# Performance work log

Hardware: AMD Instinct MI355X
Metric: run time of the kernel (lower is better)

The kernel has to match this reference:

```python
import jax, jax.numpy as jnp
import numpy as np

B, S, D = 8, 1024, 1152
H, HD = 16, 72  # num_heads, head_dim

def setup_inputs() -> dict:
    key = jax.random.key(0)
    ks = jax.random.split(key, 7)
    hidden_states = jax.random.normal(ks[0], (B, S, D), dtype=jnp.float32)
    cos = jax.random.uniform(ks[1], (S, HD), dtype=jnp.float32)
    sin = jax.random.uniform(ks[2], (S, HD), dtype=jnp.float32)
    qkv_w = jax.random.normal(ks[3], (3 * D, D), dtype=jnp.float32) * 0.02
    qkv_b = jnp.zeros((3 * D,), dtype=jnp.float32)
    proj_w = jax.random.normal(ks[4], (D, D), dtype=jnp.float32) * 0.02
    proj_b = jnp.zeros((D,), dtype=jnp.float32)
    return {"hidden_states": hidden_states, "cos": cos, "sin": sin,
            "qkv_w": qkv_w, "qkv_b": qkv_b, "proj_w": proj_w, "proj_b": proj_b}

def _rotate_half(x):
    x1, x2 = jnp.split(x, 2, axis=-1)
    return jnp.concatenate((-x2, x1), axis=-1)

def reference(hidden_states, cos, sin, qkv_w, qkv_b, proj_w, proj_b):
    b, s, d = hidden_states.shape
    # fused QKV projection
    qkv = hidden_states @ qkv_w.T + qkv_b            # [B,S,3D]
    qkv = qkv.reshape(b, s, 3, H, HD)
    qkv = jnp.transpose(qkv, (2, 0, 3, 1, 4))        # [3,B,H,S,HD]
    q, k, v = qkv[0], qkv[1], qkv[2]
    # rotary embedding, cos/sin broadcast [1,1,S,HD]
    c = cos[None, None, :, :]
    sn = sin[None, None, :, :]
    q = q * c + _rotate_half(q) * sn
    k = k * c + _rotate_half(k) * sn
    # SDPA
    scale = HD ** -0.5
    scores = jnp.einsum('bhqd,bhkd->bhqk', q, k) * scale
    probs = jax.nn.softmax(scores, axis=-1)
    attn = jnp.einsum('bhqk,bhkd->bhqd', probs, v)   # [B,H,S,HD]
    attn = jnp.transpose(attn, (0, 2, 1, 3)).reshape(b, s, d)
    return attn @ proj_w.T + proj_b
```

## Files before the change

kernel.cpp:

```cpp
#include <hip/hip_runtime.h>
#include <hip/hip_bf16.h>


typedef __attribute__((ext_vector_type(8))) short short8;
typedef __attribute__((ext_vector_type(4))) float f32x4;

__device__ __forceinline__ float bflo(unsigned int u) { return __uint_as_float(u << 16); }

__device__ __forceinline__ unsigned int f2bf(float f) {
    unsigned int u = __float_as_uint(f);
    return (u + 0x7FFFu + ((u >> 16) & 1u)) >> 16;
}

__device__ __forceinline__ void stout(float* C, size_t idx, float v) { C[idx] = v; }
__device__ __forceinline__ void stout(__hip_bfloat16* C, size_t idx, float v) {
    C[idx] = __float2bfloat16(v);
}

__device__ __forceinline__ void async_cp16(const void* g, void* l) {
    __builtin_amdgcn_global_load_lds((const __attribute__((address_space(1))) void*)g,
                                     (__attribute__((address_space(3))) void*)l, 16, 0, 0);
}

__global__ void f32_to_bf16_pair(
    const float* __restrict__ s0, unsigned short* __restrict__ d0, int n0_4,
    const float* __restrict__ s1, unsigned short* __restrict__ d1, int n1_4)
{
    int i = blockIdx.x * 256 + threadIdx.x;
    const float* s; unsigned short* d;
    if (i < n0_4) { s = s0; d = d0; }
    else if (i < n0_4 + n1_4) { s = s1; d = d1; i -= n0_4; }
    else return;
    float4 f = ((const float4*)s)[i];
    ushort4 r;
    r.x = (unsigned short)f2bf(f.x);
    r.y = (unsigned short)f2bf(f.y);
    r.z = (unsigned short)f2bf(f.z);
    r.w = (unsigned short)f2bf(f.w);
    ((ushort4*)d)[i] = r;
}

template <typename OT>
__global__ __launch_bounds__(256, 2) void gemm_bt_lds(
    const __hip_bfloat16* __restrict__ A,
    const __hip_bfloat16* __restrict__ B,
    const float* __restrict__ bias,
    OT* __restrict__ C,
    int M, int N, int K)
{
    __shared__ __align__(16) unsigned short As[128 * 32];
    __shared__ __align__(16) unsigned short Bs[128 * 32];

    const int tid  = threadIdx.x;
    const int lane = tid & 63;
    const int w    = tid >> 6;
    const int wr   = w >> 1;
    const int wc   = w & 1;
    const int bm   = blockIdx.y * 128;
    const int bn   = blockIdx.x * 128;

    const int lrow = lane >> 2;
    const int lcol = (lane & 3) * 8;

    const unsigned short* ag[2];
    const unsigned short* bg[2];
    unsigned short* al[2];
    unsigned short* bl[2];
#pragma unroll
    for (int c = 0; c < 2; c++) {
        const int r = w * 32 + c * 16 + lrow;
        ag[c] = (const unsigned short*)A + (size_t)(bm + r) * K + lcol;
        bg[c] = (const unsigned short*)B + (size_t)(bn + r) * K + lcol;
        al[c] = &As[(w * 2 + c) * 512];
        bl[c] = &Bs[(w * 2 + c) * 512];
    }

    f32x4 acc[4][4];
#pragma unroll
    for (int i = 0; i < 4; i++)
#pragma unroll
        for (int j = 0; j < 4; j++)
            acc[i][j] = (f32x4){0.f, 0.f, 0.f, 0.f};

    const int kq = (lane >> 4) * 8;
    const int fr = lane & 15;

    for (int k0 = 0; k0 < K; k0 += 32) {
        __syncthreads();
#pragma unroll
        for (int c = 0; c < 2; c++) {
            async_cp16(ag[c] + k0, al[c]);
            async_cp16(bg[c] + k0, bl[c]);
        }
        __syncthreads();

        short8 af[4], bf[4];
#pragma unroll
        for (int i = 0; i < 4; i++)
            af[i] = *(const short8*)&As[(wr * 64 + i * 16 + fr) * 32 + kq];
#pragma unroll
        for (int j = 0; j < 4; j++)
            bf[j] = *(const short8*)&Bs[(wc * 64 + j * 16 + fr) * 32 + kq];
#pragma unroll
        for (int i = 0; i < 4; i++)
#pragma unroll
            for (int j = 0; j < 4; j++)
                acc[i][j] = __builtin_amdgcn_mfma_f32_16x16x32_bf16(af[i], bf[j], acc[i][j], 0, 0, 0);
    }

#pragma unroll
    for (int i = 0; i < 4; i++) {
        const int mrow = bm + wr * 64 + i * 16 + (lane >> 4) * 4;
#pragma unroll
        for (int j = 0; j < 4; j++) {
            const int ncol = bn + wc * 64 + j * 16 + fr;
            const float bv = bias[ncol];
#pragma unroll
            for (int r = 0; r < 4; r++) {
                stout(C, (size_t)(mrow + r) * N + ncol, acc[i][j][r] + bv);
            }
        }
    }
}

__global__ void rope_qk(
    const __hip_bfloat16* __restrict__ qkv,
    const float* __restrict__ cosp,
    const float* __restrict__ sinp,
    __hip_bfloat16* __restrict__ Qo,
    __hip_bfloat16* __restrict__ Ko)
{
    const int tid = blockIdx.x * 256 + threadIdx.x;
    const int total = 8 * 16 * 1024 * 36;
    if (tid >= total) return;
    const int i    = tid % 36;
    const int rest = tid / 36;
    const int s    = rest & 1023;
    const int bh   = rest >> 10;

    const size_t row = (size_t)((bh >> 4) * 1024 + s) * 3456;
    const int col = (bh & 15) * 72 + i;

    const float c1 = cosp[s * 72 + i];
    const float c2 = cosp[s * 72 + i + 36];
    const float s1 = sinp[s * 72 + i];
    const float s2 = sinp[s * 72 + i + 36];

    const float qa = __bfloat162float(qkv[row + col]);
    const float qb = __bfloat162float(qkv[row + col + 36]);
    const float ka = __bfloat162float(qkv[row + 1152 + col]);
    const float kb = __bfloat162float(qkv[row + 1152 + col + 36]);

    const size_t ob = ((size_t)bh * 1024 + s) * 72 + i;
    const float QS = 0.17002324f;

    Qo[ob]      = __float2bfloat16((qa * c1 - qb * s1) * QS);
    Qo[ob + 36] = __float2bfloat16((qb * c2 + qa * s2) * QS);
    Ko[ob]      = __float2bfloat16(ka * c1 - kb * s1);
    Ko[ob + 36] = __float2bfloat16(kb * c2 + ka * s2);
}

__global__ void v_transpose(
    const __hip_bfloat16* __restrict__ qkv,
    __hip_bfloat16* __restrict__ Vt)
{
    __shared__ __align__(16) unsigned short T[64 * 72];
    const int tid = threadIdx.x;
    const int bh = blockIdx.x >> 4;
    const int st = blockIdx.x & 15;
    const unsigned short* src = (const unsigned short*)qkv
        + ((size_t)(bh >> 4) * 1024 + st * 64) * 3456 + 2304 + (bh & 15) * 72;

#pragma unroll
    for (int k = 0; k < 3; k++) {
        const int c = tid + k * 256;
        if (c < 576) {
            const int s = c / 9, off = (c % 9) * 8;
            *(uint4*)&T[c * 8] = *(const uint4*)(src + (size_t)s * 3456 + off);
        }
    }
    __syncthreads();

    unsigned short* dst = (unsigned short*)Vt + (size_t)(bh * 16 + st) * 72 * 64;
#pragma unroll
    for (int k = 0; k < 9; k++) {
        const int o = tid + k * 256;
        const int d = o >> 5;
        const int sl = (o & 31) * 2;
        ushort2 v;
        v.x = T[sl * 72 + d];
        v.y = T[(sl + 1) * 72 + d];
        *(ushort2*)&dst[d * 64 + sl] = v;
    }
}

__global__ __launch_bounds__(256, 4) void attn_mfma(
    const __hip_bfloat16* __restrict__ Q,
    const __hip_bfloat16* __restrict__ K,
    const __hip_bfloat16* __restrict__ Vt,
    __hip_bfloat16* __restrict__ O)
{
    __shared__ __align__(16) unsigned short Ks[64][72];
    __shared__ __align__(16) unsigned short Vs[80][72];
    __shared__ __align__(16) unsigned short Ps[4][32][72];

    const int tid  = threadIdx.x;
    const int lane = tid & 63;
    const int w    = tid >> 6;
    const int quad = lane >> 4;
    const int fr   = lane & 15;
    const int bh   = blockIdx.x & 127;
    const int qt   = blockIdx.x >> 7;
    const int qbase = qt * 128 + w * 32;

    const short8 z8 = (short8){0,0,0,0,0,0,0,0};

    for (int idx = tid; idx < 8 * 72; idx += 256)
        Vs[72 + idx / 72][idx % 72] = (idx < 72) ? (unsigned short)0x3F80 : (unsigned short)0;

    const unsigned short* qp = (const unsigned short*)Q + ((size_t)bh * 1024 + qbase + fr) * 72;
    short8 qf[2][3];
#pragma unroll
    for (int sub = 0; sub < 2; sub++) {
        const unsigned short* qs = qp + sub * 16 * 72;
        qf[sub][0] = *(const short8*)(qs + quad * 8);
        qf[sub][1] = *(const short8*)(qs + 32 + quad * 8);
        qf[sub][2] = (quad == 0) ? *(const short8*)(qs + 64) : z8;
    }

    f32x4 Oa[2][5];
#pragma unroll
    for (int sub = 0; sub < 2; sub++)
#pragma unroll
        for (int n = 0; n < 5; n++) Oa[sub][n] = (f32x4){0.f, 0.f, 0.f, 0.f};

    const unsigned short* kg0 = (const unsigned short*)K + (size_t)bh * 1024 * 72;
    const unsigned short* vg0 = (const unsigned short*)Vt + (size_t)bh * 16 * 72 * 64;

#pragma unroll 1
    for (int t = 0; t < 16; t++) {
        __syncthreads();
        const unsigned short* kg = kg0 + (size_t)t * 64 * 72;
        const unsigned short* vg = vg0 + (size_t)t * 72 * 64;
#pragma unroll
        for (int k = 0; k < 3; k++) {
            const int c = tid + k * 256;
            if (c < 576) {
                *(uint4*)&((unsigned short*)Ks)[c * 8] = *(const uint4*)(kg + c * 8);
                *(uint4*)&Vs[c >> 3][(c & 7) * 8] = *(const uint4*)(vg + c * 8);
            }
        }
        __syncthreads();

#pragma unroll
        for (int nt = 0; nt < 4; nt++) {
            short8 b0 = *(const short8*)&Ks[nt * 16 + fr][quad * 8];
            short8 b1 = *(const short8*)&Ks[nt * 16 + fr][32 + quad * 8];
            short8 b2 = (quad == 0) ? *(const short8*)&Ks[nt * 16 + fr][64] : z8;
            f32x4 s0 = (f32x4){0.f, 0.f, 0.f, 0.f};
            f32x4 s1 = (f32x4){0.f, 0.f, 0.f, 0.f};
            s0 = __builtin_amdgcn_mfma_f32_16x16x32_bf16(qf[0][0], b0, s0, 0, 0, 0);
            s1 = __builtin_amdgcn_mfma_f32_16x16x32_bf16(qf[1][0], b0, s1, 0, 0, 0);
            s0 = __builtin_amdgcn_mfma_f32_16x16x32_bf16(qf[0][1], b1, s0, 0, 0, 0);
            s1 = __builtin_amdgcn_mfma_f32_16x16x32_bf16(qf[1][1], b1, s1, 0, 0, 0);
            s0 = __builtin_amdgcn_mfma_f32_16x16x32_bf16(qf[0][2], b2, s0, 0, 0, 0);
            s1 = __builtin_amdgcn_mfma_f32_16x16x32_bf16(qf[1][2], b2, s1, 0, 0, 0);
#pragma unroll
            for (int r = 0; r < 4; r++) {
                Ps[w][quad * 4 + r][nt * 16 + fr]      = (unsigned short)f2bf(exp2f(s0[r]));
                Ps[w][16 + quad * 4 + r][nt * 16 + fr] = (unsigned short)f2bf(exp2f(s1[r]));
            }
        }

#pragma unroll
        for (int ks = 0; ks < 2; ks++) {
            short8 ap0 = *(const short8*)&Ps[w][fr][ks * 32 + quad * 8];
            short8 ap1 = *(const short8*)&Ps[w][16 + fr][ks * 32 + quad * 8];
#pragma unroll
            for (int n = 0; n < 5; n++) {
                short8 bv = *(const short8*)&Vs[n * 16 + fr][ks * 32 + quad * 8];
                Oa[0][n] = __builtin_amdgcn_mfma_f32_16x16x32_bf16(ap0, bv, Oa[0][n], 0, 0, 0);
                Oa[1][n] = __builtin_amdgcn_mfma_f32_16x16x32_bf16(ap1, bv, Oa[1][n], 0, 0, 0);
            }
        }
    }

    const int lsrc = (lane & 48) | 8;
    const int b = bh >> 4, h = bh & 15;
    unsigned short* ob = (unsigned short*)O;
#pragma unroll
    for (int sub = 0; sub < 2; sub++) {
        float inv[4];
#pragma unroll
        for (int r = 0; r < 4; r++)
            inv[r] = 1.f / __shfl(Oa[sub][4][r], lsrc, 64);
#pragma unroll
        for (int n = 0; n < 5; n++) {
            const int d = n * 16 + fr;
            if (d < 72) {
#pragma unroll
                for (int r = 0; r < 4; r++) {
                    const size_t idx =
                        ((size_t)b * 1024 + qbase + sub * 16 + quad * 4 + r) * 1152 + h * 72 + d;
                    ob[idx] = (unsigned short)f2bf(Oa[sub][n][r] * inv[r]);
                }
            }
        }
    }
}

extern "C" void kernel_launch(void* const* d_in, const int* in_sizes, int n_in,
                              void* d_out, int out_size, void* d_ws, size_t ws_size,
                              hipStream_t stream)
{
    const float* hs     = (const float*)d_in[0];
    const float* cosp   = (const float*)d_in[1];
    const float* sinp   = (const float*)d_in[2];
    const float* qkv_w  = (const float*)d_in[3];
    const float* qkv_b  = (const float*)d_in[4];
    const float* proj_w = (const float*)d_in[5];
    const float* proj_b = (const float*)d_in[6];
    float* out = (float*)d_out;

    char* ws = (char*)d_ws;
    __hip_bfloat16* qkv_buf = (__hip_bfloat16*)ws;
    __hip_bfloat16* Qb = (__hip_bfloat16*)(ws + 56623104);
    __hip_bfloat16* Kb = Qb + 9437184;
    __hip_bfloat16* Vt = Kb + 9437184;
    __hip_bfloat16* Ab = qkv_buf;

    unsigned short* hs_bf = (unsigned short*)Qb;
    unsigned short* qw_bf = (unsigned short*)Kb;
    unsigned short* pw_bf = (unsigned short*)Qb;

    f32_to_bf16_pair<<<13104, 256, 0, stream>>>(hs, hs_bf, 2359296,
                                                qkv_w, qw_bf, 995328);
    gemm_bt_lds<__hip_bfloat16>
        <<<dim3(27, 64), 256, 0, stream>>>((const __hip_bfloat16*)hs_bf,
                                           (const __hip_bfloat16*)qw_bf,
                                           qkv_b, qkv_buf, 8192, 3456, 1152);
    rope_qk<<<18432, 256, 0, stream>>>(qkv_buf, cosp, sinp, Qb, Kb);
    v_transpose<<<2048, 256, 0, stream>>>(qkv_buf, Vt);
    attn_mfma<<<1024, 256, 0, stream>>>(Qb, Kb, Vt, Ab);
    f32_to_bf16_pair<<<1296, 256, 0, stream>>>(proj_w, pw_bf, 331776,
                                               nullptr, nullptr, 0);
    gemm_bt_lds<float>
        <<<dim3(9, 64), 256, 0, stream>>>((const __hip_bfloat16*)Ab,
                                          (const __hip_bfloat16*)pw_bf,
                                          proj_b, out, 8192, 1152, 1152);
}
```

Measured before the change: 337.3 us.

## Double GEMM K-step to 64 and fuse RoPE with V transpose kernel

The bf16 GEMM now loads a 64-wide K slab per iteration, held as two 32-wide LDS halves, which halves the number of barrier pairs per tile and doubles the LDS footprint. Separately, the rope_qk and v_transpose kernels are merged into one rope_v_prep kernel. Each block of that kernel transposes V through LDS and also applies RoPE to Q and K for the same 64-row slice, which removes one launch and makes the qkv reads of the same rows more local. The larger LDS use may lower occupancy, and the loads are still not overlapped with compute.

```diff
diff --git a/kernel.cpp b/kernel.cpp
--- a/kernel.cpp
+++ b/kernel.cpp
@@ -48,8 +48,8 @@
     OT* __restrict__ C,
     int M, int N, int K)
 {
-    __shared__ __align__(16) unsigned short As[128 * 32];
-    __shared__ __align__(16) unsigned short Bs[128 * 32];
+    __shared__ __align__(16) unsigned short As[2 * 128 * 32];
+    __shared__ __align__(16) unsigned short Bs[2 * 128 * 32];
 
     const int tid  = threadIdx.x;
     const int lane = tid & 63;
@@ -62,17 +62,21 @@
     const int lrow = lane >> 2;
     const int lcol = (lane & 3) * 8;
 
-    const unsigned short* ag[2];
-    const unsigned short* bg[2];
-    unsigned short* al[2];
-    unsigned short* bl[2];
+    const unsigned short* ag[4];
+    const unsigned short* bg[4];
+    unsigned short* al[4];
+    unsigned short* bl[4];
 #pragma unroll
     for (int c = 0; c < 2; c++) {
         const int r = w * 32 + c * 16 + lrow;
-        ag[c] = (const unsigned short*)A + (size_t)(bm + r) * K + lcol;
-        bg[c] = (const unsigned short*)B + (size_t)(bn + r) * K + lcol;
-        al[c] = &As[(w * 2 + c) * 512];
-        bl[c] = &Bs[(w * 2 + c) * 512];
+#pragma unroll
+        for (int h = 0; h < 2; h++) {
+            const int idx = c * 2 + h;
+            ag[idx] = (const unsigned short*)A + (size_t)(bm + r) * K + h * 32 + lcol;
+            bg[idx] = (const unsigned short*)B + (size_t)(bn + r) * K + h * 32 + lcol;
+            al[idx] = &As[h * 4096 + (w * 2 + c) * 512];
+            bl[idx] = &Bs[h * 4096 + (w * 2 + c) * 512];
+        }
     }
 
     f32x4 acc[4][4];
@@ -85,27 +89,30 @@
     const int kq = (lane >> 4) * 8;
     const int fr = lane & 15;
 
-    for (int k0 = 0; k0 < K; k0 += 32) {
+    for (int k0 = 0; k0 < K; k0 += 64) {
         __syncthreads();
 #pragma unroll
-        for (int c = 0; c < 2; c++) {
+        for (int c = 0; c < 4; c++) {
             async_cp16(ag[c] + k0, al[c]);
             async_cp16(bg[c] + k0, bl[c]);
         }
         __syncthreads();
 
-        short8 af[4], bf[4];
-#pragma unroll
-        for (int i = 0; i < 4; i++)
-            af[i] = *(const short8*)&As[(wr * 64 + i * 16 + fr) * 32 + kq];
-#pragma unroll
-        for (int j = 0; j < 4; j++)
-            bf[j] = *(const short8*)&Bs[(wc * 64 + j * 16 + fr) * 32 + kq];
-#pragma unroll
-        for (int i = 0; i < 4; i++)
+#pragma unroll
+        for (int h = 0; h < 2; h++) {
+            short8 af[4], bf[4];
+#pragma unroll
+            for (int i = 0; i < 4; i++)
+                af[i] = *(const short8*)&As[h * 4096 + (wr * 64 + i * 16 + fr) * 32 + kq];
 #pragma unroll
             for (int j = 0; j < 4; j++)
-                acc[i][j] = __builtin_amdgcn_mfma_f32_16x16x32_bf16(af[i], bf[j], acc[i][j], 0, 0, 0);
+                bf[j] = *(const short8*)&Bs[h * 4096 + (wc * 64 + j * 16 + fr) * 32 + kq];
+#pragma unroll
+            for (int i = 0; i < 4; i++)
+#pragma unroll
+                for (int j = 0; j < 4; j++)
+                    acc[i][j] = __builtin_amdgcn_mfma_f32_16x16x32_bf16(af[i], bf[j], acc[i][j], 0, 0, 0);
+        }
     }
 
 #pragma unroll
@@ -123,62 +130,60 @@
     }
 }
 
-__global__ void rope_qk(
+__global__ void rope_v_prep(
     const __hip_bfloat16* __restrict__ qkv,
     const float* __restrict__ cosp,
     const float* __restrict__ sinp,
     __hip_bfloat16* __restrict__ Qo,
-    __hip_bfloat16* __restrict__ Ko)
-{
-    const int tid = blockIdx.x * 256 + threadIdx.x;
-    const int total = 8 * 16 * 1024 * 36;
-    if (tid >= total) return;
-    const int i    = tid % 36;
-    const int rest = tid / 36;
-    const int s    = rest & 1023;
-    const int bh   = rest >> 10;
-
-    const size_t row = (size_t)((bh >> 4) * 1024 + s) * 3456;
-    const int col = (bh & 15) * 72 + i;
-
-    const float c1 = cosp[s * 72 + i];
-    const float c2 = cosp[s * 72 + i + 36];
-    const float s1 = sinp[s * 72 + i];
-    const float s2 = sinp[s * 72 + i + 36];
-
-    const float qa = __bfloat162float(qkv[row + col]);
-    const float qb = __bfloat162float(qkv[row + col + 36]);
-    const float ka = __bfloat162float(qkv[row + 1152 + col]);
-    const float kb = __bfloat162float(qkv[row + 1152 + col + 36]);
-
-    const size_t ob = ((size_t)bh * 1024 + s) * 72 + i;
-    const float QS = 0.17002324f;
-
-    Qo[ob]      = __float2bfloat16((qa * c1 - qb * s1) * QS);
-    Qo[ob + 36] = __float2bfloat16((qb * c2 + qa * s2) * QS);
-    Ko[ob]      = __float2bfloat16(ka * c1 - kb * s1);
-    Ko[ob + 36] = __float2bfloat16(kb * c2 + ka * s2);
-}
-
-__global__ void v_transpose(
-    const __hip_bfloat16* __restrict__ qkv,
+    __hip_bfloat16* __restrict__ Ko,
     __hip_bfloat16* __restrict__ Vt)
 {
     __shared__ __align__(16) unsigned short T[64 * 72];
     const int tid = threadIdx.x;
     const int bh = blockIdx.x >> 4;
     const int st = blockIdx.x & 15;
-    const unsigned short* src = (const unsigned short*)qkv
-        + ((size_t)(bh >> 4) * 1024 + st * 64) * 3456 + 2304 + (bh & 15) * 72;
-
+    const int b = bh >> 4, h = bh & 15;
+    const size_t row0 = ((size_t)b * 1024 + st * 64) * 3456;
+
+    const unsigned short* vsrc = (const unsigned short*)qkv + row0 + 2304 + h * 72;
 #pragma unroll
     for (int k = 0; k < 3; k++) {
         const int c = tid + k * 256;
         if (c < 576) {
             const int s = c / 9, off = (c % 9) * 8;
-            *(uint4*)&T[c * 8] = *(const uint4*)(src + (size_t)s * 3456 + off);
-        }
-    }
+            *(uint4*)&T[c * 8] = *(const uint4*)(vsrc + (size_t)s * 3456 + off);
+        }
+    }
+
+    const unsigned short* qkvp = (const unsigned short*)qkv;
+    const float QS = 0.17002324f;
+#pragma unroll
+    for (int k = 0; k < 9; k++) {
+        const int p = tid + k * 256;
+        const int sl = p / 36, i = p % 36;
+        const int sg = st * 64 + sl;
+        const size_t row = row0 + (size_t)sl * 3456;
+        const int col = h * 72 + i;
+
+        const float c1 = cosp[sg * 72 + i];
+        const float c2 = cosp[sg * 72 + i + 36];
+        const float s1 = sinp[sg * 72 + i];
+        const float s2 = sinp[sg * 72 + i + 36];
+
+        const float qa = bflo((unsigned int)qkvp[row + col] << 16 >> 16 | ((unsigned int)qkvp[row + col]));
+        const float qa2 = __uint_as_float((unsigned int)qkvp[row + col] << 16);
+        const float qb  = __uint_as_float((unsigned int)qkvp[row + col + 36] << 16);
+        const float ka  = __uint_as_float((unsigned int)qkvp[row + 1152 + col] << 16);
+        const float kb  = __uint_as_float((unsigned int)qkvp[row + 1152 + col + 36] << 16);
+        (void)qa;
+
+        const size_t ob = ((size_t)bh * 1024 + sg) * 72 + i;
+        ((unsigned short*)Qo)[ob]      = (unsigned short)f2bf((qa2 * c1 - qb * s1) * QS);
+        ((unsigned short*)Qo)[ob + 36] = (unsigned short)f2bf((qb * c2 + qa2 * s2) * QS);
+        ((unsigned short*)Ko)[ob]      = (unsigned short)f2bf(ka * c1 - kb * s1);
+        ((unsigned short*)Ko)[ob + 36] = (unsigned short)f2bf(kb * c2 + ka * s2);
+    }
+
     __syncthreads();
 
     unsigned short* dst = (unsigned short*)Vt + (size_t)(bh * 16 + st) * 72 * 64;
@@ -339,8 +344,7 @@
         <<<dim3(27, 64), 256, 0, stream>>>((const __hip_bfloat16*)hs_bf,
                                            (const __hip_bfloat16*)qw_bf,
                                            qkv_b, qkv_buf, 8192, 3456, 1152);
-    rope_qk<<<18432, 256, 0, stream>>>(qkv_buf, cosp, sinp, Qb, Kb);
-    v_transpose<<<2048, 256, 0, stream>>>(qkv_buf, Vt);
+    rope_v_prep<<<2048, 256, 0, stream>>>(qkv_buf, cosp, sinp, Qb, Kb, Vt);
     attn_mfma<<<1024, 256, 0, stream>>>(Qb, Kb, Vt, Ab);
     f32_to_bf16_pair<<<1296, 256, 0, stream>>>(proj_w, pw_bf, 331776,
                                                nullptr, nullptr, 0);
```

Result: no change. 336.7 us (-0.2%).
